# Kernel optimization log

Measured on AMD Instinct MI355X. Metric: run time of the kernel, lower is better.

## Reference

```python
import jax, jax.numpy as jnp
import numpy as np

B, S, D, H = 4, 512, 1024, 16
HD = D // H
K_TOP = 8
MC_K = 8
EPS6 = 1e-6


def _affine(loc, scale, W, b):
    # Gaussian-diag affine: mu = x@W.T+b, var = scale^2 @ (W^2).T
    mu = loc @ W.T + b
    var = (scale ** 2) @ (W ** 2).T
    return mu, jnp.sqrt(var)


def _split(x):  # [B,S,D] -> [B,H,S,HD]
    return x.reshape(B, S, H, HD).transpose(0, 2, 1, 3)


def _combine(x):  # [B,H,S,HD] -> [B,S,D]
    return x.transpose(0, 2, 1, 3).reshape(B, S, D)


def _softmax_logit_normal(mu, var, excl_mask):
    # logit-normal softmax moment approximation (probit / delta method),
    # excluding masked positions (prob -> 0 there).
    adj = mu / jnp.sqrt(1.0 + (jnp.pi / 8.0) * var)
    adj = jnp.where(excl_mask, -1e9, adj)
    p = jax.nn.softmax(adj, axis=-1)
    v = (p * (1.0 - p)) ** 2 * var
    return p, v


def _forward(Q_loc, Q_scale, K_loc, K_scale, V_loc, V_scale,
             Wq, bq, Wk, bk, Wv, bv, Wo, bo, tau, eps):
    q_mu, q_sc = _affine(Q_loc, Q_scale, Wq, bq)
    k_mu, k_sc = _affine(K_loc, K_scale, Wk, bk)
    v_mu, v_sc = _affine(V_loc, V_scale, Wv, bv)

    # split heads; GaussianDiag round-trip adds 1e-6 to scale before squaring
    qm, qv = _split(q_mu), (_split(q_sc) + EPS6) ** 2
    km, kv = _split(k_mu), (_split(k_sc) + EPS6) ** 2
    vm, vv = _split(v_mu), (_split(v_sc) + EPS6) ** 2

    # bilinear moment: E[QK^T], Var[QK^T]
    S_mu = jnp.einsum('bhqd,bhkd->bhqk', qm, km)
    S_var = (jnp.einsum('bhqd,bhkd->bhqk', qm ** 2, kv)
             + jnp.einsum('bhqd,bhkd->bhqk', qv, km ** 2)
             + jnp.einsum('bhqd,bhkd->bhqk', qv, kv)) + EPS6

    s_mu = S_mu / jnp.sqrt(jnp.float32(HD))
    s_var = S_var / HD + EPS6

    l_mu = s_mu / tau
    l_var = s_var / (tau ** 2) + EPS6

    # top-k indices by mean logit
    topk_idx = jax.lax.top_k(l_mu, K_TOP)[1]  # [B,H,S,K_TOP]
    rows = jnp.arange(B * H * S)[:, None]
    mask = jnp.zeros((B * H * S, S), bool).at[rows, topk_idx.reshape(-1, K_TOP)].set(True)
    mask = mask.reshape(B, H, S, S)

    # MC-sample softmax (mc_k=8)
    std = jnp.sqrt(jnp.maximum(l_var, 1e-9))
    p_mean = jax.nn.softmax(l_mu[None] + std[None] * eps, axis=-1).mean(axis=0)

    # rest (non-top-k) logit-normal softmax moments
    rest_mean, rest_var = _softmax_logit_normal(l_mu, l_var, mask)

    top_out = jnp.where(mask, p_mean, rest_mean)
    top_out = top_out / jnp.maximum(top_out.sum(axis=-1, keepdims=True), 1e-12)

    # combine_top_rest: means add (variances do not feed the output path)
    attn_mu = top_out + rest_mean

    # linear combination with V distribution
    Y_mu = jnp.einsum('bhqk,bhkd->bhqd', attn_mu, vm)
    Y_var = jnp.einsum('bhqk,bhkd->bhqd', attn_mu ** 2, vv)
    Y_scale = jnp.sqrt(Y_var + EPS6)

    y_loc = _combine(Y_mu)
    y_scale = _combine(Y_scale) + EPS6

    out_loc = y_loc @ Wo.T + bo
    out_scale = jnp.sqrt((y_scale ** 2) @ (Wo ** 2).T)
    return out_loc, out_scale


def setup_inputs() -> dict:
    key = jax.random.key(0)
    ks = jax.random.split(key, 17)
    f32 = jnp.float32
    inp = {
        'Q_loc': jax.random.normal(ks[0], (B, S, D), f32),
        'Q_scale': jax.random.uniform(ks[1], (B, S, D), f32),
        'K_loc': jax.random.normal(ks[2], (B, S, D), f32),
        'K_scale': jax.random.uniform(ks[3], (B, S, D), f32),
        'V_loc': jax.random.normal(ks[4], (B, S, D), f32),
        'V_scale': jax.random.uniform(ks[5], (B, S, D), f32),
        'Wq': jax.random.normal(ks[6], (D, D), f32) * 0.02,
        'bq': jnp.zeros((D,), f32),
        'Wk': jax.random.normal(ks[7], (D, D), f32) * 0.02,
        'bk': jnp.zeros((D,), f32),
        'Wv': jax.random.normal(ks[8], (D, D), f32) * 0.02,
        'bv': jnp.zeros((D,), f32),
        'Wo': jax.random.normal(ks[9], (D, D), f32) * 0.02,
        'bo': jnp.zeros((D,), f32),
        'tau': jnp.array(1.0, f32),
        'eps': jax.random.normal(ks[10], (MC_K, B, H, S, S), f32),
    }
    return inp


def reference(Q_loc, Q_scale, K_loc, K_scale, V_loc, V_scale,
              Wq, bq, Wk, bk, Wv, bv, Wo, bo, tau, eps):
    return _forward(Q_loc, Q_scale, K_loc, K_scale, V_loc, V_scale,
                    Wq, bq, Wk, bk, Wv, bv, Wo, bo, tau, eps)
```

## Files before the change

### kernel.cpp

```cpp
#include <hip/hip_runtime.h>
#include <math.h>

#define B_ 4
#define S_ 512
#define D_ 1024
#define H_ 16
#define MCK 8
#define MS 2048
#define BHSS_ ((size_t)16777216)
#define BHS_  ((size_t)32768)

typedef __attribute__((ext_vector_type(8))) __bf16 bf16x8;
typedef __attribute__((ext_vector_type(4))) __bf16 bf16x4;
typedef __attribute__((ext_vector_type(4))) float f32x4;

__device__ __forceinline__ f32x4 mfma16(bf16x8 a, bf16x8 b, f32x4 c) {
  return __builtin_amdgcn_mfma_f32_16x16x32_bf16(a, b, c, 0, 0, 0);
}
__device__ __forceinline__ bf16x8 sq8(bf16x8 x) {
  bf16x8 r;
#pragma unroll
  for (int i = 0; i < 8; ++i) { float f = (float)x[i]; r[i] = (__bf16)(f * f); }
  return r;
}
__device__ __forceinline__ float wave_max(float v) {
#pragma unroll
  for (int o = 32; o; o >>= 1) v = fmaxf(v, __shfl_xor(v, o));
  return v;
}
__device__ __forceinline__ float wave_sum(float v) {
#pragma unroll
  for (int o = 32; o; o >>= 1) v += __shfl_xor(v, o);
  return v;
}

__global__ __launch_bounds__(256) void conv_ls(
    const float* __restrict__ l0, const float* __restrict__ s0,
    const float* __restrict__ l1, const float* __restrict__ s1,
    const float* __restrict__ l2, const float* __restrict__ s2,
    __bf16* h0, __bf16* o0, __bf16* v0,
    __bf16* h1, __bf16* o1, __bf16* v1,
    __bf16* h2, __bf16* o2, __bf16* v2)
{
  const int tn = blockIdx.x >> 10;
  const size_t i0 = ((size_t)(blockIdx.x & 1023) * 256 + threadIdx.x) * 8;
  const float* L = tn == 0 ? l0 : tn == 1 ? l1 : l2;
  const float* S = tn == 0 ? s0 : tn == 1 ? s1 : s2;
  __bf16* Hh = tn == 0 ? h0 : tn == 1 ? h1 : h2;
  __bf16* Lo = tn == 0 ? o0 : tn == 1 ? o1 : o2;
  __bf16* V2 = tn == 0 ? v0 : tn == 1 ? v1 : v2;
  float4 x0 = *(const float4*)(L + i0), x1 = *(const float4*)(L + i0 + 4);
  float4 y0 = *(const float4*)(S + i0), y1 = *(const float4*)(S + i0 + 4);
  float xs[8] = {x0.x, x0.y, x0.z, x0.w, x1.x, x1.y, x1.z, x1.w};
  float ys[8] = {y0.x, y0.y, y0.z, y0.w, y1.x, y1.y, y1.z, y1.w};
  bf16x8 hh, ll, vv;
#pragma unroll
  for (int i = 0; i < 8; ++i) {
    __bf16 h = (__bf16)xs[i];
    hh[i] = h;
    ll[i] = (__bf16)(xs[i] - (float)h);
    vv[i] = (__bf16)(ys[i] * ys[i]);
  }
  *(bf16x8*)(Hh + i0) = hh;
  *(bf16x8*)(Lo + i0) = ll;
  *(bf16x8*)(V2 + i0) = vv;
}

__global__ __launch_bounds__(256) void conv_w(
    const float* __restrict__ w0, const float* __restrict__ w1,
    const float* __restrict__ w2, const float* __restrict__ w3,
    __bf16* h0, __bf16* o0, __bf16* q0,
    __bf16* h1, __bf16* o1, __bf16* q1,
    __bf16* h2, __bf16* o2, __bf16* q2,
    __bf16* h3, __bf16* o3, __bf16* q3)
{
  const int tn = blockIdx.x >> 9;
  const size_t i0 = ((size_t)(blockIdx.x & 511) * 256 + threadIdx.x) * 8;
  const float* W = tn == 0 ? w0 : tn == 1 ? w1 : tn == 2 ? w2 : w3;
  __bf16* Hh = tn == 0 ? h0 : tn == 1 ? h1 : tn == 2 ? h2 : h3;
  __bf16* Lo = tn == 0 ? o0 : tn == 1 ? o1 : tn == 2 ? o2 : o3;
  __bf16* Qq = tn == 0 ? q0 : tn == 1 ? q1 : tn == 2 ? q2 : q3;
  float4 x0 = *(const float4*)(W + i0), x1 = *(const float4*)(W + i0 + 4);
  float xs[8] = {x0.x, x0.y, x0.z, x0.w, x1.x, x1.y, x1.z, x1.w};
  bf16x8 hh, ll, qq;
#pragma unroll
  for (int i = 0; i < 8; ++i) {
    __bf16 h = (__bf16)xs[i];
    hh[i] = h;
    ll[i] = (__bf16)(xs[i] - (float)h);
    qq[i] = (__bf16)(xs[i] * xs[i]);
  }
  *(bf16x8*)(Hh + i0) = hh;
  *(bf16x8*)(Lo + i0) = ll;
  *(bf16x8*)(Qq + i0) = qq;
}

template<int EPI>
__global__ __launch_bounds__(256) void dgemm(
    const __bf16* __restrict__ Ah, const __bf16* __restrict__ Al, const __bf16* __restrict__ A2,
    const __bf16* __restrict__ Wh, const __bf16* __restrict__ Wl, const __bf16* __restrict__ W2,
    const float* __restrict__ bias,
    void* __restrict__ P0, void* __restrict__ P1, void* __restrict__ P2, void* __restrict__ P3)
{
  __shared__ __bf16 sA[3][64][32];
  __shared__ __bf16 sW[3][64][32];
  const int t = threadIdx.x;
  const int lane = t & 63, wid = t >> 6;
  const int wm = wid >> 1, wn = wid & 1;
  const int m0 = blockIdx.y * 64, n0 = blockIdx.x * 64;
  f32x4 accM[2][2] = {}; f32x4 accV[2][2] = {};
  const int crow = t >> 2, ccol = (t & 3) * 8;
  for (int k0 = 0; k0 < D_; k0 += 32) {
    size_t ga = (size_t)(m0 + crow) * D_ + k0 + ccol;
    size_t gw = (size_t)(n0 + crow) * D_ + k0 + ccol;
    bf16x8 va0 = *(const bf16x8*)(Ah + ga);
    bf16x8 va1 = *(const bf16x8*)(Al + ga);
    bf16x8 va2 = *(const bf16x8*)(A2 + ga);
    bf16x8 vw0 = *(const bf16x8*)(Wh + gw);
    bf16x8 vw1 = *(const bf16x8*)(Wl + gw);
    bf16x8 vw2 = *(const bf16x8*)(W2 + gw);
    __syncthreads();
    *(bf16x8*)&sA[0][crow][ccol] = va0;
    *(bf16x8*)&sA[1][crow][ccol] = va1;
    *(bf16x8*)&sA[2][crow][ccol] = va2;
    *(bf16x8*)&sW[0][crow][ccol] = vw0;
    *(bf16x8*)&sW[1][crow][ccol] = vw1;
    *(bf16x8*)&sW[2][crow][ccol] = vw2;
    __syncthreads();
    const int fr = lane & 15, kc = (lane >> 4) * 8;
    bf16x8 fah[2], fal[2], fa2[2];
#pragma unroll
    for (int i = 0; i < 2; ++i) {
      int r = wm * 32 + i * 16 + fr;
      fah[i] = *(const bf16x8*)&sA[0][r][kc];
      fal[i] = *(const bf16x8*)&sA[1][r][kc];
      fa2[i] = *(const bf16x8*)&sA[2][r][kc];
    }
#pragma unroll
    for (int j = 0; j < 2; ++j) {
      int r = wn * 32 + j * 16 + fr;
      bf16x8 fwh = *(const bf16x8*)&sW[0][r][kc];
      bf16x8 fwl = *(const bf16x8*)&sW[1][r][kc];
      bf16x8 fw2 = *(const bf16x8*)&sW[2][r][kc];
#pragma unroll
      for (int i = 0; i < 2; ++i) {
        accM[i][j] = mfma16(fah[i], fwh, accM[i][j]);
        accM[i][j] = mfma16(fah[i], fwl, accM[i][j]);
        accM[i][j] = mfma16(fal[i], fwh, accM[i][j]);
        accV[i][j] = mfma16(fa2[i], fw2, accV[i][j]);
      }
    }
  }
  const int fr = lane & 15, fq = lane >> 4;
#pragma unroll
  for (int i = 0; i < 2; ++i)
#pragma unroll
    for (int j = 0; j < 2; ++j) {
      const int col = n0 + wn * 32 + j * 16 + fr;
      const int row0 = m0 + wm * 32 + i * 16 + fq * 4;
      f32x4 m_ = accM[i][j], v_ = accV[i][j];
      const float bcol = bias[col];
      if (EPI == 0) {
#pragma unroll
        for (int r = 0; r < 4; ++r) {
          size_t off = (size_t)(row0 + r) * D_ + col;
          float mu = m_[r] + bcol;
          __bf16 h = (__bf16)mu;
          float s = sqrtf(v_[r]) + 1e-6f;
          ((__bf16*)P0)[off] = h;
          ((__bf16*)P1)[off] = (__bf16)(mu - (float)h);
          ((__bf16*)P2)[off] = (__bf16)(mu * mu);
          ((__bf16*)P3)[off] = (__bf16)(s * s);
        }
      } else if (EPI == 1) {
        const int b = row0 >> 9, ss0 = row0 & 511;
        const int hh = col >> 6, dd = col & 63;
        size_t base = ((size_t)(b * H_ + hh) * 64 + dd) * S_ + ss0;
        bf16x4 vh, vl, vq;
#pragma unroll
        for (int r = 0; r < 4; ++r) {
          float mu = m_[r] + bcol;
          __bf16 h = (__bf16)mu;
          vh[r] = h;
          vl[r] = (__bf16)(mu - (float)h);
          float s = sqrtf(v_[r]) + 1e-6f;
          vq[r] = (__bf16)(s * s);
        }
        *(bf16x4*)((__bf16*)P0 + base) = vh;
        *(bf16x4*)((__bf16*)P1 + base) = vl;
        *(bf16x4*)((__bf16*)P2 + base) = vq;
      } else {
#pragma unroll
        for (int r = 0; r < 4; ++r) {
          size_t off = (size_t)(row0 + r) * D_ + col;
          ((float*)P0)[off] = m_[r] + bcol;
          ((float*)P1)[off] = sqrtf(v_[r]);
        }
      }
    }
}

__global__ __launch_bounds__(256) void score_mfma(
    const __bf16* __restrict__ qh, const __bf16* __restrict__ ql,
    const __bf16* __restrict__ q2, const __bf16* __restrict__ qv,
    const __bf16* __restrict__ kh, const __bf16* __restrict__ kl,
    const __bf16* __restrict__ k2, const __bf16* __restrict__ kv,
    float* __restrict__ lmu, __bf16* __restrict__ lvar,
    const float* __restrict__ taup)
{
  __shared__ __bf16 sQ[4][64][32];
  __shared__ __bf16 sK[4][64][32];
  const int t = threadIdx.x;
  const int lane = t & 63, wid = t >> 6;
  const int wm = wid >> 1, wn = wid & 1;
  const int kk0 = blockIdx.x * 64, q0 = blockIdx.y * 64, bh = blockIdx.z;
  const int b = bh >> 4, h = bh & 15;
  const size_t hb = ((size_t)b * S_) * D_ + (size_t)h * 64;
  f32x4 accM[2][2] = {}; f32x4 accV[2][2] = {};
  const int crow = t >> 2, ccol = (t & 3) * 8;
  for (int d0 = 0; d0 < 64; d0 += 32) {
    size_t gq = hb + (size_t)(q0 + crow) * D_ + d0 + ccol;
    size_t gk = hb + (size_t)(kk0 + crow) * D_ + d0 + ccol;
    bf16x8 a0 = *(const bf16x8*)(qh + gq);
    bf16x8 a1 = *(const bf16x8*)(ql + gq);
    bf16x8 a2 = *(const bf16x8*)(q2 + gq);
    bf16x8 a3 = *(const bf16x8*)(qv + gq);
    bf16x8 b0 = *(const bf16x8*)(kh + gk);
    bf16x8 b1 = *(const bf16x8*)(kl + gk);
    bf16x8 b2 = *(const bf16x8*)(k2 + gk);
    bf16x8 b3 = *(const bf16x8*)(kv + gk);
    __syncthreads();
    *(bf16x8*)&sQ[0][crow][ccol] = a0;
    *(bf16x8*)&sQ[1][crow][ccol] = a1;
    *(bf16x8*)&sQ[2][crow][ccol] = a2;
    *(bf16x8*)&sQ[3][crow][ccol] = a3;
    *(bf16x8*)&sK[0][crow][ccol] = b0;
    *(bf16x8*)&sK[1][crow][ccol] = b1;
    *(bf16x8*)&sK[2][crow][ccol] = b2;
    *(bf16x8*)&sK[3][crow][ccol] = b3;
    __syncthreads();
    const int fr = lane & 15, kc = (lane >> 4) * 8;
    bf16x8 fqh[2], fql[2], fq2[2], fqv[2];
#pragma unroll
    for (int i = 0; i < 2; ++i) {
      int r = wm * 32 + i * 16 + fr;
      fqh[i] = *(const bf16x8*)&sQ[0][r][kc];
      fql[i] = *(const bf16x8*)&sQ[1][r][kc];
      fq2[i] = *(const bf16x8*)&sQ[2][r][kc];
      fqv[i] = *(const bf16x8*)&sQ[3][r][kc];
    }
#pragma unroll
    for (int j = 0; j < 2; ++j) {
      int r = wn * 32 + j * 16 + fr;
      bf16x8 fkh = *(const bf16x8*)&sK[0][r][kc];
      bf16x8 fkl = *(const bf16x8*)&sK[1][r][kc];
      bf16x8 fk2 = *(const bf16x8*)&sK[2][r][kc];
      bf16x8 fkv = *(const bf16x8*)&sK[3][r][kc];
#pragma unroll
      for (int i = 0; i < 2; ++i) {
        accM[i][j] = mfma16(fqh[i], fkh, accM[i][j]);
        accM[i][j] = mfma16(fqh[i], fkl, accM[i][j]);
        accM[i][j] = mfma16(fql[i], fkh, accM[i][j]);
        accV[i][j] = mfma16(fq2[i], fkv, accV[i][j]);
        accV[i][j] = mfma16(fqv[i], fk2, accV[i][j]);
        accV[i][j] = mfma16(fqv[i], fkv, accV[i][j]);
      }
    }
  }
  const float itau = 1.0f / *taup;
  const int fr = lane & 15, fq = lane >> 4;
#pragma unroll
  for (int i = 0; i < 2; ++i)
#pragma unroll
    for (int j = 0; j < 2; ++j) {
      const int col = kk0 + wn * 32 + j * 16 + fr;
      const int row0 = q0 + wm * 32 + i * 16 + fq * 4;
      f32x4 m_ = accM[i][j], v_ = accV[i][j];
#pragma unroll
      for (int r = 0; r < 4; ++r) {
        size_t off = ((size_t)bh * S_ + row0 + r) * S_ + col;
        lmu[off] = m_[r] * 0.125f * itau;
        float lv = ((v_[r] + 1e-6f) * (1.0f / 64.0f) + 1e-6f) * itau * itau + 1e-6f;
        lvar[off] = (__bf16)lv;
      }
    }
}

__global__ __launch_bounds__(256) void attn_kernel(
    const float* __restrict__ lmu, const __bf16* __restrict__ lvar,
    const float* __restrict__ eps, __bf16* __restrict__ ah, __bf16* __restrict__ al)
{
  const int wid = threadIdx.x >> 6;
  const int lane = threadIdx.x & 63;
  const size_t r = (size_t)blockIdx.x * 4 + wid;
  const float* mrow = lmu + r * S_;
  const __bf16* vrow = lvar + r * S_;
  float mu[8], va[8], sd[8];
#pragma unroll
  for (int i = 0; i < 8; ++i) {
    mu[i] = mrow[lane + 64 * i];
    va[i] = (float)vrow[lane + 64 * i];
    sd[i] = sqrtf(fmaxf(va[i], 1e-9f));
  }
  unsigned sel = 0;
  float x[8];
#pragma unroll
  for (int i = 0; i < 8; ++i) x[i] = mu[i];
  for (int tsel = 0; tsel < 8; ++tsel) {
    float bv = -INFINITY; int bi = 0x7fffffff;
#pragma unroll
    for (int i = 0; i < 8; ++i) {
      int gi = lane + 64 * i;
      if (x[i] > bv || (x[i] == bv && gi < bi)) { bv = x[i]; bi = gi; }
    }
    for (int o = 32; o; o >>= 1) {
      float ov = __shfl_xor(bv, o); int oi = __shfl_xor(bi, o);
      if (ov > bv || (ov == bv && oi < bi)) { bv = ov; bi = oi; }
    }
    if ((bi & 63) == lane) { sel |= 1u << (bi >> 6); x[bi >> 6] = -INFINITY; }
  }
  float pacc[8] = {0, 0, 0, 0, 0, 0, 0, 0};
  for (int mc = 0; mc < MCK; ++mc) {
    const float* ep = eps + (size_t)mc * BHSS_ + r * S_ + lane;
    float xv[8];
#pragma unroll
    for (int i = 0; i < 8; ++i) xv[i] = mu[i] + sd[i] * ep[64 * i];
    float m = -INFINITY;
#pragma unroll
    for (int i = 0; i < 8; ++i) m = fmaxf(m, xv[i]);
    m = wave_max(m);
    float e[8], zs = 0.f;
#pragma unroll
    for (int i = 0; i < 8; ++i) { e[i] = __expf(xv[i] - m); zs += e[i]; }
    zs = wave_sum(zs);
    float inv = 1.0f / zs;
#pragma unroll
    for (int i = 0; i < 8; ++i) pacc[i] += e[i] * inv;
  }
  float adj[8];
#pragma unroll
  for (int i = 0; i < 8; ++i) {
    float a = mu[i] / sqrtf(1.0f + 0.39269908169872414f * va[i]);
    adj[i] = ((sel >> i) & 1u) ? -1e9f : a;
  }
  float m2 = -INFINITY;
#pragma unroll
  for (int i = 0; i < 8; ++i) m2 = fmaxf(m2, adj[i]);
  m2 = wave_max(m2);
  float e2[8], z2 = 0.f;
#pragma unroll
  for (int i = 0; i < 8; ++i) { e2[i] = __expf(adj[i] - m2); z2 += e2[i]; }
  z2 = wave_sum(z2);
  float inv2 = 1.0f / z2;
  float rest[8], tout[8], s = 0.f;
#pragma unroll
  for (int i = 0; i < 8; ++i) {
    rest[i] = e2[i] * inv2;
    tout[i] = ((sel >> i) & 1u) ? pacc[i] * 0.125f : rest[i];
    s += tout[i];
  }
  s = wave_sum(s);
  float rn = 1.0f / fmaxf(s, 1e-12f);
#pragma unroll
  for (int i = 0; i < 8; ++i) {
    float o = tout[i] * rn + rest[i];
    __bf16 h = (__bf16)o;
    ah[r * S_ + lane + 64 * i] = h;
    al[r * S_ + lane + 64 * i] = (__bf16)(o - (float)h);
  }
}

__global__ __launch_bounds__(256) void pv_mfma(
    const __bf16* __restrict__ ah_, const __bf16* __restrict__ al_,
    const __bf16* __restrict__ vTh, const __bf16* __restrict__ vTl,
    const __bf16* __restrict__ vTv,
    __bf16* __restrict__ yh, __bf16* __restrict__ yl, __bf16* __restrict__ ys2)
{
  __shared__ __bf16 sA[2][64][32];
  __shared__ __bf16 sV[3][64][32];
  const int t = threadIdx.x;
  const int lane = t & 63, wid = t >> 6;
  const int wm = wid >> 1, wn = wid & 1;
  const int q0 = blockIdx.x * 64, bh = blockIdx.y;
  const int b = bh >> 4, h = bh & 15;
  const __bf16* Ah = ah_ + (size_t)bh * S_ * S_;
  const __bf16* Al = al_ + (size_t)bh * S_ * S_;
  const __bf16* Vh = vTh + (size_t)bh * 64 * S_;
  const __bf16* Vl = vTl + (size_t)bh * 64 * S_;
  const __bf16* Vv = vTv + (size_t)bh * 64 * S_;
  f32x4 accM[2][2] = {}; f32x4 accV[2][2] = {};
  const int crow = t >> 2, ccol = (t & 3) * 8;
  for (int k0 = 0; k0 < S_; k0 += 32) {
    size_t gA = (size_t)(q0 + crow) * S_ + k0 + ccol;
    size_t gV = (size_t)crow * S_ + k0 + ccol;
    bf16x8 a0 = *(const bf16x8*)(Ah + gA);
    bf16x8 a1 = *(const bf16x8*)(Al + gA);
    bf16x8 v0 = *(const bf16x8*)(Vh + gV);
    bf16x8 v1 = *(const bf16x8*)(Vl + gV);
    bf16x8 v2 = *(const bf16x8*)(Vv + gV);
    __syncthreads();
    *(bf16x8*)&sA[0][crow][ccol] = a0;
    *(bf16x8*)&sA[1][crow][ccol] = a1;
    *(bf16x8*)&sV[0][crow][ccol] = v0;
    *(bf16x8*)&sV[1][crow][ccol] = v1;
    *(bf16x8*)&sV[2][crow][ccol] = v2;
    __syncthreads();
    const int fr = lane & 15, kc = (lane >> 4) * 8;
    bf16x8 fah[2], fal[2], fa2[2];
#pragma unroll
    for (int i = 0; i < 2; ++i) {
      int rr = wm * 32 + i * 16 + fr;
      fah[i] = *(const bf16x8*)&sA[0][rr][kc];
      fal[i] = *(const bf16x8*)&sA[1][rr][kc];
      fa2[i] = sq8(fah[i]);
    }
#pragma unroll
    for (int j = 0; j < 2; ++j) {
      int rr = wn * 32 + j * 16 + fr;
      bf16x8 fvh = *(const bf16x8*)&sV[0][rr][kc];
      bf16x8 fvl = *(const bf16x8*)&sV[1][rr][kc];
      bf16x8 fvv = *(const bf16x8*)&sV[2][rr][kc];
#pragma unroll
      for (int i = 0; i < 2; ++i) {
        accM[i][j] = mfma16(fah[i], fvh, accM[i][j]);
        accM[i][j] = mfma16(fah[i], fvl, accM[i][j]);
        accM[i][j] = mfma16(fal[i], fvh, accM[i][j]);
        accV[i][j] = mfma16(fa2[i], fvv, accV[i][j]);
      }
    }
  }
  const int fr = lane & 15, fq = lane >> 4;
#pragma unroll
  for (int i = 0; i < 2; ++i)
#pragma unroll
    for (int j = 0; j < 2; ++j) {
      const int col = h * 64 + wn * 32 + j * 16 + fr;
      const int row0 = b * S_ + q0 + wm * 32 + i * 16 + fq * 4;
      f32x4 m_ = accM[i][j], v_ = accV[i][j];
#pragma unroll
      for (int r = 0; r < 4; ++r) {
        size_t off = (size_t)(row0 + r) * D_ + col;
        float mu = m_[r];
        __bf16 hh = (__bf16)mu;
        float ss = sqrtf(v_[r] + 1e-6f) + 1e-6f;
        yh[off] = hh;
        yl[off] = (__bf16)(mu - (float)hh);
        ys2[off] = (__bf16)(ss * ss);
      }
    }
}

extern "C" void kernel_launch(void* const* d_in, const int* in_sizes, int n_in,
                              void* d_out, int out_size, void* d_ws, size_t ws_size,
                              hipStream_t stream)
{
  const float* Qloc = (const float*)d_in[0];
  const float* Qsc  = (const float*)d_in[1];
  const float* Kloc = (const float*)d_in[2];
  const float* Ksc  = (const float*)d_in[3];
  const float* Vloc = (const float*)d_in[4];
  const float* Vsc  = (const float*)d_in[5];
  const float* Wq = (const float*)d_in[6];  const float* bq = (const float*)d_in[7];
  const float* Wk = (const float*)d_in[8];  const float* bk = (const float*)d_in[9];
  const float* Wv = (const float*)d_in[10]; const float* bv = (const float*)d_in[11];
  const float* Wo = (const float*)d_in[12]; const float* bo = (const float*)d_in[13];
  const float* tau = (const float*)d_in[14];
  const float* eps = (const float*)d_in[15];

  const size_t P = (size_t)MS * D_;
  const size_t DD = (size_t)D_ * D_;
  char* w = (char*)d_ws;
  auto carve = [&](size_t bytes) -> char* {
    char* p = w; w += (bytes + 255) & ~(size_t)255; return p;
  };
  __bf16* cQh = (__bf16*)carve(P * 2); __bf16* cQl = (__bf16*)carve(P * 2); __bf16* cQ2 = (__bf16*)carve(P * 2);
  __bf16* cKh = (__bf16*)carve(P * 2); __bf16* cKl = (__bf16*)carve(P * 2); __bf16* cK2 = (__bf16*)carve(P * 2);
  __bf16* cVh = (__bf16*)carve(P * 2); __bf16* cVl = (__bf16*)carve(P * 2); __bf16* cV2 = (__bf16*)carve(P * 2);
  __bf16* wqh = (__bf16*)carve(DD * 2); __bf16* wql = (__bf16*)carve(DD * 2); __bf16* wq2 = (__bf16*)carve(DD * 2);
  __bf16* wkh = (__bf16*)carve(DD * 2); __bf16* wkl = (__bf16*)carve(DD * 2); __bf16* wk2 = (__bf16*)carve(DD * 2);
  __bf16* wvh = (__bf16*)carve(DD * 2); __bf16* wvl = (__bf16*)carve(DD * 2); __bf16* wv2 = (__bf16*)carve(DD * 2);
  __bf16* woh = (__bf16*)carve(DD * 2); __bf16* wol = (__bf16*)carve(DD * 2); __bf16* wo2 = (__bf16*)carve(DD * 2);
  __bf16* qmh = (__bf16*)carve(P * 2); __bf16* qml = (__bf16*)carve(P * 2);
  __bf16* qm2 = (__bf16*)carve(P * 2); __bf16* qmv = (__bf16*)carve(P * 2);
  __bf16* kmh = (__bf16*)carve(P * 2); __bf16* kml = (__bf16*)carve(P * 2);
  __bf16* km2 = (__bf16*)carve(P * 2); __bf16* kmv = (__bf16*)carve(P * 2);
  __bf16* vTh = (__bf16*)carve(P * 2); __bf16* vTl = (__bf16*)carve(P * 2); __bf16* vTv = (__bf16*)carve(P * 2);
  float*  lmu = (float*)carve(BHSS_ * 4);
  __bf16* lvr = (__bf16*)carve(BHSS_ * 2);
  __bf16* ath = (__bf16*)carve(BHSS_ * 2);
  __bf16* atl = (__bf16*)carve(BHSS_ * 2);
  __bf16* yh = (__bf16*)carve(P * 2); __bf16* yl = (__bf16*)carve(P * 2); __bf16* ys2 = (__bf16*)carve(P * 2);
  float* out_loc = (float*)d_out;
  float* out_sc  = out_loc + P;

  dim3 blk(256);
  conv_ls<<<3 * 1024, blk, 0, stream>>>(Qloc, Qsc, Kloc, Ksc, Vloc, Vsc,
                                        cQh, cQl, cQ2, cKh, cKl, cK2, cVh, cVl, cV2);
  conv_w<<<4 * 512, blk, 0, stream>>>(Wq, Wk, Wv, Wo,
                                      wqh, wql, wq2, wkh, wkl, wk2,
                                      wvh, wvl, wv2, woh, wol, wo2);
  dim3 gG(16, 32);
  dgemm<0><<<gG, blk, 0, stream>>>(cQh, cQl, cQ2, wqh, wql, wq2, bq, qmh, qml, qm2, qmv);
  dgemm<0><<<gG, blk, 0, stream>>>(cKh, cKl, cK2, wkh, wkl, wk2, bk, kmh, kml, km2, kmv);
  dgemm<1><<<gG, blk, 0, stream>>>(cVh, cVl, cV2, wvh, wvl, wv2, bv, vTh, vTl, vTv, nullptr);
  score_mfma<<<dim3(8, 8, 64), blk, 0, stream>>>(qmh, qml, qm2, qmv, kmh, kml, km2, kmv, lmu, lvr, tau);
  attn_kernel<<<dim3((unsigned)(BHS_ / 4)), blk, 0, stream>>>(lmu, lvr, eps, ath, atl);
  pv_mfma<<<dim3(8, 64), blk, 0, stream>>>(ath, atl, vTh, vTl, vTv, yh, yl, ys2);
  dgemm<2><<<gG, blk, 0, stream>>>(yh, yl, ys2, woh, wol, wo2, bo, out_loc, out_sc, nullptr, nullptr);
}
```

Measured before the change: 403.5 us.

## Merge QKV projections into one launch with larger swizzled LDS-direct tiles

Replaces the three separate projection GEMMs with one batched launch indexed by blockIdx.z, and widens each block's tile to 64x128. Global loads now go straight into XOR-swizzled LDS through global_load_lds, which removes the register staging and the bank conflicts. The squared-weight operand is no longer precomputed and stored; it is recomputed in-kernel as (hi+lo)^2, which saves conv_w writes and W2 reads at the cost of extra ALU work. The output GEMM gets the same restructuring. The larger per-thread accumulator count may raise register pressure and lower occupancy.

```diff
diff --git a/kernel.cpp b/kernel.cpp
--- a/kernel.cpp
+++ b/kernel.cpp
@@ -23,6 +23,12 @@
   for (int i = 0; i < 8; ++i) { float f = (float)x[i]; r[i] = (__bf16)(f * f); }
   return r;
 }
+__device__ __forceinline__ bf16x8 sq8s(bf16x8 h, bf16x8 l) {
+  bf16x8 r;
+#pragma unroll
+  for (int i = 0; i < 8; ++i) { float f = (float)h[i] + (float)l[i]; r[i] = (__bf16)(f * f); }
+  return r;
+}
 __device__ __forceinline__ float wave_max(float v) {
 #pragma unroll
   for (int o = 32; o; o >>= 1) v = fmaxf(v, __shfl_xor(v, o));
@@ -32,6 +38,22 @@
 #pragma unroll
   for (int o = 32; o; o >>= 1) v += __shfl_xor(v, o);
   return v;
+}
+
+__device__ __forceinline__ void unswz(int u, int& row, int& slot) {
+  int row0 = ((u >> 2) ^ (u >> 4)) & 1;
+  row = ((u >> 3) << 1) | row0;
+  int s0 = (u ^ (u >> 2) ^ (u >> 4)) & 1;
+  int s1 = ((u >> 1) ^ (u >> 3)) & 1;
+  slot = (s1 << 1) | s0;
+}
+__device__ __forceinline__ int swz_el(int row, int slot) {
+  return ((row * 4 + slot) ^ (row & 7)) * 8;
+}
+__device__ __forceinline__ void glds16(const void* gsrc, void* ldst) {
+  __builtin_amdgcn_global_load_lds(
+      (const __attribute__((address_space(1))) void*)gsrc,
+      (__attribute__((address_space(3))) void*)ldst, 16, 0, 0);
 }
 
 __global__ __launch_bounds__(256) void conv_ls(
@@ -69,81 +91,75 @@
 __global__ __launch_bounds__(256) void conv_w(
     const float* __restrict__ w0, const float* __restrict__ w1,
     const float* __restrict__ w2, const float* __restrict__ w3,
-    __bf16* h0, __bf16* o0, __bf16* q0,
-    __bf16* h1, __bf16* o1, __bf16* q1,
-    __bf16* h2, __bf16* o2, __bf16* q2,
-    __bf16* h3, __bf16* o3, __bf16* q3)
+    __bf16* h0, __bf16* o0, __bf16* h1, __bf16* o1,
+    __bf16* h2, __bf16* o2, __bf16* h3, __bf16* o3)
 {
   const int tn = blockIdx.x >> 9;
   const size_t i0 = ((size_t)(blockIdx.x & 511) * 256 + threadIdx.x) * 8;
   const float* W = tn == 0 ? w0 : tn == 1 ? w1 : tn == 2 ? w2 : w3;
   __bf16* Hh = tn == 0 ? h0 : tn == 1 ? h1 : tn == 2 ? h2 : h3;
   __bf16* Lo = tn == 0 ? o0 : tn == 1 ? o1 : tn == 2 ? o2 : o3;
-  __bf16* Qq = tn == 0 ? q0 : tn == 1 ? q1 : tn == 2 ? q2 : q3;
   float4 x0 = *(const float4*)(W + i0), x1 = *(const float4*)(W + i0 + 4);
   float xs[8] = {x0.x, x0.y, x0.z, x0.w, x1.x, x1.y, x1.z, x1.w};
-  bf16x8 hh, ll, qq;
+  bf16x8 hh, ll;
 #pragma unroll
   for (int i = 0; i < 8; ++i) {
     __bf16 h = (__bf16)xs[i];
     hh[i] = h;
     ll[i] = (__bf16)(xs[i] - (float)h);
-    qq[i] = (__bf16)(xs[i] * xs[i]);
   }
   *(bf16x8*)(Hh + i0) = hh;
   *(bf16x8*)(Lo + i0) = ll;
-  *(bf16x8*)(Qq + i0) = qq;
-}
-
-template<int EPI>
-__global__ __launch_bounds__(256) void dgemm(
-    const __bf16* __restrict__ Ah, const __bf16* __restrict__ Al, const __bf16* __restrict__ A2,
-    const __bf16* __restrict__ Wh, const __bf16* __restrict__ Wl, const __bf16* __restrict__ W2,
-    const float* __restrict__ bias,
-    void* __restrict__ P0, void* __restrict__ P1, void* __restrict__ P2, void* __restrict__ P3)
-{
-  __shared__ __bf16 sA[3][64][32];
-  __shared__ __bf16 sW[3][64][32];
-  const int t = threadIdx.x;
-  const int lane = t & 63, wid = t >> 6;
-  const int wm = wid >> 1, wn = wid & 1;
-  const int m0 = blockIdx.y * 64, n0 = blockIdx.x * 64;
-  f32x4 accM[2][2] = {}; f32x4 accV[2][2] = {};
-  const int crow = t >> 2, ccol = (t & 3) * 8;
+}
+
+struct PArg {
+  const __bf16 *Ah, *Al, *A2, *Wh, *Wl;
+  const float* bias;
+  __bf16 *P0, *P1, *P2, *P3;
+  int epi;
+};
+struct PArg3 { PArg a[3]; };
+
+__global__ __launch_bounds__(256, 3) void dgemm_qkv(PArg3 P3v)
+{
+  __shared__ __bf16 lds[14336];
+  const PArg p = P3v.a[blockIdx.z];
+  const int t = threadIdx.x, lane = t & 63, wid = t >> 6;
+  const int m0 = blockIdx.y * 64, n0 = blockIdx.x * 128;
+  int rA, sA; unswz(t, rA, sA);
+  const size_t gA = (size_t)(m0 + rA) * D_ + sA * 8;
+  const size_t gW0 = (size_t)(n0 + rA) * D_ + sA * 8;
+  int rW1, sW1; unswz(t + 256, rW1, sW1);
+  const size_t gW1 = (size_t)(n0 + rW1) * D_ + sW1 * 8;
+  const int wofs = wid * 512;
+  f32x4 accM[4][2] = {}; f32x4 accV[4][2] = {};
+  const int fr = lane & 15, ks = lane >> 4;
   for (int k0 = 0; k0 < D_; k0 += 32) {
-    size_t ga = (size_t)(m0 + crow) * D_ + k0 + ccol;
-    size_t gw = (size_t)(n0 + crow) * D_ + k0 + ccol;
-    bf16x8 va0 = *(const bf16x8*)(Ah + ga);
-    bf16x8 va1 = *(const bf16x8*)(Al + ga);
-    bf16x8 va2 = *(const bf16x8*)(A2 + ga);
-    bf16x8 vw0 = *(const bf16x8*)(Wh + gw);
-    bf16x8 vw1 = *(const bf16x8*)(Wl + gw);
-    bf16x8 vw2 = *(const bf16x8*)(W2 + gw);
+    if (k0) __syncthreads();
+    glds16(p.Ah + gA + k0,  lds + 0     + wofs);
+    glds16(p.Al + gA + k0,  lds + 2048  + wofs);
+    glds16(p.A2 + gA + k0,  lds + 4096  + wofs);
+    glds16(p.Wh + gW0 + k0, lds + 6144  + wofs);
+    glds16(p.Wl + gW0 + k0, lds + 10240 + wofs);
+    glds16(p.Wh + gW1 + k0, lds + 6144 + 2048 + wofs);
+    glds16(p.Wl + gW1 + k0, lds + 10240 + 2048 + wofs);
     __syncthreads();
-    *(bf16x8*)&sA[0][crow][ccol] = va0;
-    *(bf16x8*)&sA[1][crow][ccol] = va1;
-    *(bf16x8*)&sA[2][crow][ccol] = va2;
-    *(bf16x8*)&sW[0][crow][ccol] = vw0;
-    *(bf16x8*)&sW[1][crow][ccol] = vw1;
-    *(bf16x8*)&sW[2][crow][ccol] = vw2;
-    __syncthreads();
-    const int fr = lane & 15, kc = (lane >> 4) * 8;
-    bf16x8 fah[2], fal[2], fa2[2];
-#pragma unroll
-    for (int i = 0; i < 2; ++i) {
-      int r = wm * 32 + i * 16 + fr;
-      fah[i] = *(const bf16x8*)&sA[0][r][kc];
-      fal[i] = *(const bf16x8*)&sA[1][r][kc];
-      fa2[i] = *(const bf16x8*)&sA[2][r][kc];
+    bf16x8 fah[4], fal[4], fa2[4];
+#pragma unroll
+    for (int i = 0; i < 4; ++i) {
+      int so = swz_el(i * 16 + fr, ks);
+      fah[i] = *(const bf16x8*)(lds + 0 + so);
+      fal[i] = *(const bf16x8*)(lds + 2048 + so);
+      fa2[i] = *(const bf16x8*)(lds + 4096 + so);
     }
 #pragma unroll
     for (int j = 0; j < 2; ++j) {
-      int r = wn * 32 + j * 16 + fr;
-      bf16x8 fwh = *(const bf16x8*)&sW[0][r][kc];
-      bf16x8 fwl = *(const bf16x8*)&sW[1][r][kc];
-      bf16x8 fw2 = *(const bf16x8*)&sW[2][r][kc];
-#pragma unroll
-      for (int i = 0; i < 2; ++i) {
+      int so = swz_el(wid * 32 + j * 16 + fr, ks);
+      bf16x8 fwh = *(const bf16x8*)(lds + 6144 + so);
+      bf16x8 fwl = *(const bf16x8*)(lds + 10240 + so);
+      bf16x8 fw2 = sq8s(fwh, fwl);
+#pragma unroll
+      for (int i = 0; i < 4; ++i) {
         accM[i][j] = mfma16(fah[i], fwh, accM[i][j]);
         accM[i][j] = mfma16(fah[i], fwl, accM[i][j]);
         accM[i][j] = mfma16(fal[i], fwh, accM[i][j]);
@@ -151,28 +167,28 @@
       }
     }
   }
-  const int fr = lane & 15, fq = lane >> 4;
-#pragma unroll
-  for (int i = 0; i < 2; ++i)
-#pragma unroll
-    for (int j = 0; j < 2; ++j) {
-      const int col = n0 + wn * 32 + j * 16 + fr;
-      const int row0 = m0 + wm * 32 + i * 16 + fq * 4;
+  const int fq = lane >> 4;
+#pragma unroll
+  for (int j = 0; j < 2; ++j) {
+    const int col = n0 + wid * 32 + j * 16 + fr;
+    const float bcol = p.bias[col];
+#pragma unroll
+    for (int i = 0; i < 4; ++i) {
+      const int row0 = m0 + i * 16 + fq * 4;
       f32x4 m_ = accM[i][j], v_ = accV[i][j];
-      const float bcol = bias[col];
-      if (EPI == 0) {
+      if (p.epi == 0) {
 #pragma unroll
         for (int r = 0; r < 4; ++r) {
           size_t off = (size_t)(row0 + r) * D_ + col;
           float mu = m_[r] + bcol;
           __bf16 h = (__bf16)mu;
           float s = sqrtf(v_[r]) + 1e-6f;
-          ((__bf16*)P0)[off] = h;
-          ((__bf16*)P1)[off] = (__bf16)(mu - (float)h);
-          ((__bf16*)P2)[off] = (__bf16)(mu * mu);
-          ((__bf16*)P3)[off] = (__bf16)(s * s);
+          p.P0[off] = h;
+          p.P1[off] = (__bf16)(mu - (float)h);
+          p.P2[off] = (__bf16)(mu * mu);
+          p.P3[off] = (__bf16)(s * s);
         }
-      } else if (EPI == 1) {
+      } else {
         const int b = row0 >> 9, ss0 = row0 & 511;
         const int hh = col >> 6, dd = col & 63;
         size_t base = ((size_t)(b * H_ + hh) * 64 + dd) * S_ + ss0;
@@ -186,18 +202,80 @@
           float s = sqrtf(v_[r]) + 1e-6f;
           vq[r] = (__bf16)(s * s);
         }
-        *(bf16x4*)((__bf16*)P0 + base) = vh;
-        *(bf16x4*)((__bf16*)P1 + base) = vl;
-        *(bf16x4*)((__bf16*)P2 + base) = vq;
-      } else {
-#pragma unroll
-        for (int r = 0; r < 4; ++r) {
-          size_t off = (size_t)(row0 + r) * D_ + col;
-          ((float*)P0)[off] = m_[r] + bcol;
-          ((float*)P1)[off] = sqrtf(v_[r]);
-        }
-      }
-    }
+        *(bf16x4*)(p.P0 + base) = vh;
+        *(bf16x4*)(p.P1 + base) = vl;
+        *(bf16x4*)(p.P2 + base) = vq;
+      }
+    }
+  }
+}
+
+__global__ __launch_bounds__(256) void dgemm_o(
+    const __bf16* __restrict__ Ah, const __bf16* __restrict__ Al, const __bf16* __restrict__ A2,
+    const __bf16* __restrict__ Wh, const __bf16* __restrict__ Wl,
+    const float* __restrict__ bias, float* __restrict__ O0, float* __restrict__ O1)
+{
+  __shared__ __bf16 lds[14336];
+  const int t = threadIdx.x, lane = t & 63, wid = t >> 6;
+  const int m0 = blockIdx.y * 64, n0 = blockIdx.x * 128;
+  int rA, sA; unswz(t, rA, sA);
+  const size_t gA = (size_t)(m0 + rA) * D_ + sA * 8;
+  const size_t gW0 = (size_t)(n0 + rA) * D_ + sA * 8;
+  int rW1, sW1; unswz(t + 256, rW1, sW1);
+  const size_t gW1 = (size_t)(n0 + rW1) * D_ + sW1 * 8;
+  const int wofs = wid * 512;
+  f32x4 accM[4][2] = {}; f32x4 accV[4][2] = {};
+  const int fr = lane & 15, ks = lane >> 4;
+  for (int k0 = 0; k0 < D_; k0 += 32) {
+    if (k0) __syncthreads();
+    glds16(Ah + gA + k0,  lds + 0     + wofs);
+    glds16(Al + gA + k0,  lds + 2048  + wofs);
+    glds16(A2 + gA + k0,  lds + 4096  + wofs);
+    glds16(Wh + gW0 + k0, lds + 6144  + wofs);
+    glds16(Wl + gW0 + k0, lds + 10240 + wofs);
+    glds16(Wh + gW1 + k0, lds + 6144 + 2048 + wofs);
+    glds16(Wl + gW1 + k0, lds + 10240 + 2048 + wofs);
+    __syncthreads();
+    bf16x8 fah[4], fal[4], fa2[4];
+#pragma unroll
+    for (int i = 0; i < 4; ++i) {
+      int so = swz_el(i * 16 + fr, ks);
+      fah[i] = *(const bf16x8*)(lds + 0 + so);
+      fal[i] = *(const bf16x8*)(lds + 2048 + so);
+      fa2[i] = *(const bf16x8*)(lds + 4096 + so);
+    }
+#pragma unroll
+    for (int j = 0; j < 2; ++j) {
+      int so = swz_el(wid * 32 + j * 16 + fr, ks);
+      bf16x8 fwh = *(const bf16x8*)(lds + 6144 + so);
+      bf16x8 fwl = *(const bf16x8*)(lds + 10240 + so);
+      bf16x8 fw2 = sq8s(fwh, fwl);
+#pragma unroll
+      for (int i = 0; i < 4; ++i) {
+        accM[i][j] = mfma16(fah[i], fwh, accM[i][j]);
+        accM[i][j] = mfma16(fah[i], fwl, accM[i][j]);
+        accM[i][j] = mfma16(fal[i], fwh, accM[i][j]);
+        accV[i][j] = mfma16(fa2[i], fw2, accV[i][j]);
+      }
+    }
+  }
+  const int fq = lane >> 4;
+#pragma unroll
+  for (int j = 0; j < 2; ++j) {
+    const int col = n0 + wid * 32 + j * 16 + fr;
+    const float bcol = bias[col];
+#pragma unroll
+    for (int i = 0; i < 4; ++i) {
+      const int row0 = m0 + i * 16 + fq * 4;
+      f32x4 m_ = accM[i][j], v_ = accV[i][j];
+#pragma unroll
+      for (int r = 0; r < 4; ++r) {
+        size_t off = (size_t)(row0 + r) * D_ + col;
+        O0[off] = m_[r] + bcol;
+        O1[off] = sqrtf(v_[r]);
+      }
+    }
+  }
 }
 
 __global__ __launch_bounds__(256) void score_mfma(
@@ -476,10 +554,10 @@
   __bf16* cQh = (__bf16*)carve(P * 2); __bf16* cQl = (__bf16*)carve(P * 2); __bf16* cQ2 = (__bf16*)carve(P * 2);
   __bf16* cKh = (__bf16*)carve(P * 2); __bf16* cKl = (__bf16*)carve(P * 2); __bf16* cK2 = (__bf16*)carve(P * 2);
   __bf16* cVh = (__bf16*)carve(P * 2); __bf16* cVl = (__bf16*)carve(P * 2); __bf16* cV2 = (__bf16*)carve(P * 2);
-  __bf16* wqh = (__bf16*)carve(DD * 2); __bf16* wql = (__bf16*)carve(DD * 2); __bf16* wq2 = (__bf16*)carve(DD * 2);
-  __bf16* wkh = (__bf16*)carve(DD * 2); __bf16* wkl = (__bf16*)carve(DD * 2); __bf16* wk2 = (__bf16*)carve(DD * 2);
-  __bf16* wvh = (__bf16*)carve(DD * 2); __bf16* wvl = (__bf16*)carve(DD * 2); __bf16* wv2 = (__bf16*)carve(DD * 2);
-  __bf16* woh = (__bf16*)carve(DD * 2); __bf16* wol = (__bf16*)carve(DD * 2); __bf16* wo2 = (__bf16*)carve(DD * 2);
+  __bf16* wqh = (__bf16*)carve(DD * 2); __bf16* wql = (__bf16*)carve(DD * 2);
+  __bf16* wkh = (__bf16*)carve(DD * 2); __bf16* wkl = (__bf16*)carve(DD * 2);
+  __bf16* wvh = (__bf16*)carve(DD * 2); __bf16* wvl = (__bf16*)carve(DD * 2);
+  __bf16* woh = (__bf16*)carve(DD * 2); __bf16* wol = (__bf16*)carve(DD * 2);
   __bf16* qmh = (__bf16*)carve(P * 2); __bf16* qml = (__bf16*)carve(P * 2);
   __bf16* qm2 = (__bf16*)carve(P * 2); __bf16* qmv = (__bf16*)carve(P * 2);
   __bf16* kmh = (__bf16*)carve(P * 2); __bf16* kml = (__bf16*)carve(P * 2);
@@ -497,14 +575,14 @@
   conv_ls<<<3 * 1024, blk, 0, stream>>>(Qloc, Qsc, Kloc, Ksc, Vloc, Vsc,
                                         cQh, cQl, cQ2, cKh, cKl, cK2, cVh, cVl, cV2);
   conv_w<<<4 * 512, blk, 0, stream>>>(Wq, Wk, Wv, Wo,
-                                      wqh, wql, wq2, wkh, wkl, wk2,
-                                      wvh, wvl, wv2, woh, wol, wo2);
-  dim3 gG(16, 32);
-  dgemm<0><<<gG, blk, 0, stream>>>(cQh, cQl, cQ2, wqh, wql, wq2, bq, qmh, qml, qm2, qmv);
-  dgemm<0><<<gG, blk, 0, stream>>>(cKh, cKl, cK2, wkh, wkl, wk2, bk, kmh, kml, km2, kmv);
-  dgemm<1><<<gG, blk, 0, stream>>>(cVh, cVl, cV2, wvh, wvl, wv2, bv, vTh, vTl, vTv, nullptr);
+                                      wqh, wql, wkh, wkl, wvh, wvl, woh, wol);
+  PArg3 pq;
+  pq.a[0] = PArg{cQh, cQl, cQ2, wqh, wql, bq, qmh, qml, qm2, qmv, 0};
+  pq.a[1] = PArg{cKh, cKl, cK2, wkh, wkl, bk, kmh, kml, km2, kmv, 0};
+  pq.a[2] = PArg{cVh, cVl, cV2, wvh, wvl, bv, vTh, vTl, vTv, nullptr, 1};
+  dgemm_qkv<<<dim3(8, 32, 3), blk, 0, stream>>>(pq);
   score_mfma<<<dim3(8, 8, 64), blk, 0, stream>>>(qmh, qml, qm2, qmv, kmh, kml, km2, kmv, lmu, lvr, tau);
   attn_kernel<<<dim3((unsigned)(BHS_ / 4)), blk, 0, stream>>>(lmu, lvr, eps, ath, atl);
   pv_mfma<<<dim3(8, 64), blk, 0, stream>>>(ath, atl, vTh, vTl, vTv, yh, yl, ys2);
-  dgemm<2><<<gG, blk, 0, stream>>>(yh, yl, ys2, woh, wol, wo2, bo, out_loc, out_sc, nullptr, nullptr);
-}
+  dgemm_o<<<dim3(8, 32), blk, 0, stream>>>(yh, yl, ys2, woh, wol, bo, out_loc, out_sc);
+}
```

New measurement: 390.3 us. -3.3%, faster.
